# Kernel tuning notes

Measured on AMD Instinct MI355X. Metric: run time of the kernel, lower is better.

Reference implementation:

```python
import jax, jax.numpy as jnp
import numpy as np

NUM_CLASSES = 80
STRIDES = (8, 16, 32)
PRE_TOP_K = 1000
KEEP_TOP_K = 100
IOU_THR = 0.65
SCORE_THR = 0.25
CLASS_OFFSET = 8192.0  # > max image coordinate, separates classes for batched NMS


def _make_priors_strides(featmap_sizes):
    # MlvlPointGenerator.grid_priors with offset=0 (RTMDet-style point priors)
    priors, strides = [], []
    for (h, w), s in zip(featmap_sizes, STRIDES):
        ys, xs = jnp.meshgrid(jnp.arange(h, dtype=jnp.float32) * s,
                              jnp.arange(w, dtype=jnp.float32) * s, indexing='ij')
        priors.append(jnp.stack([xs.reshape(-1), ys.reshape(-1)], axis=-1))
        strides.append(jnp.full((h * w,), float(s), dtype=jnp.float32))
    return jnp.concatenate(priors, 0), jnp.concatenate(strides, 0)


def _flatten(x, c):
    # [B, C, H, W] -> [B, H*W, c] matching permute(0,2,3,1).reshape
    b = x.shape[0]
    return jnp.transpose(x, (0, 2, 3, 1)).reshape(b, -1, c)


def _iou_matrix(boxes):
    # boxes [K, 4] x1y1x2y2 -> pairwise IoU [K, K]
    area = jnp.maximum(boxes[:, 2] - boxes[:, 0], 0.0) * jnp.maximum(boxes[:, 3] - boxes[:, 1], 0.0)
    lt = jnp.maximum(boxes[:, None, :2], boxes[None, :, :2])
    rb = jnp.minimum(boxes[:, None, 2:], boxes[None, :, 2:])
    wh = jnp.maximum(rb - lt, 0.0)
    inter = wh[..., 0] * wh[..., 1]
    return inter / jnp.maximum(area[:, None] + area[None, :] - inter, 1e-6)


def _nms_single(boxes, scores, labels):
    # boxes [N,4], scores [N] (max over classes), labels [N] int32
    valid = scores > SCORE_THR
    scores = jnp.where(valid, scores, 0.0)
    top_scores, idx = jax.lax.top_k(scores, PRE_TOP_K)  # pre_top_k filtering
    b = boxes[idx]
    lab = labels[idx]
    val = valid[idx]
    # class-aware NMS via coordinate offset per class (batched_nms trick)
    off_boxes = b + (lab.astype(b.dtype) * CLASS_OFFSET)[:, None]
    iou = _iou_matrix(off_boxes)

    def body(suppressed, i):
        keep_i = ~suppressed[i]
        suppressed = suppressed | (keep_i & (iou[i] > IOU_THR))
        suppressed = suppressed.at[i].set(~keep_i)
        return suppressed, keep_i

    _, keeps = jax.lax.scan(body, ~val, jnp.arange(PRE_TOP_K))
    final_scores = jnp.where(keeps, top_scores, 0.0)
    fs, fidx = jax.lax.top_k(final_scores, KEEP_TOP_K)
    dets = jnp.concatenate([b[fidx], fs[:, None]], axis=-1)  # [keep_top_k, 5]
    return dets, lab[fidx]


def setup_inputs() -> dict:
    key = jax.random.key(0)
    ks = jax.random.split(key, 6)
    B, C = 16, NUM_CLASSES
    return {
        'cls0': jax.random.normal(ks[0], (B, C, 80, 80), jnp.float32),
        'cls1': jax.random.normal(ks[1], (B, C, 40, 40), jnp.float32),
        'cls2': jax.random.normal(ks[2], (B, C, 20, 20), jnp.float32),
        'box0': jax.random.uniform(ks[3], (B, 4, 80, 80), jnp.float32),
        'box1': jax.random.uniform(ks[4], (B, 4, 40, 40), jnp.float32),
        'box2': jax.random.uniform(ks[5], (B, 4, 20, 20), jnp.float32),
    }


def reference(cls0, cls1, cls2, box0, box1, box2):
    featmap_sizes = [c.shape[2:] for c in (cls0, cls1, cls2)]
    priors, strides = _make_priors_strides(featmap_sizes)  # [A,2], [A]
    scores = jax.nn.sigmoid(
        jnp.concatenate([_flatten(c, NUM_CLASSES) for c in (cls0, cls1, cls2)], axis=1))  # [B,A,C]
    preds = jnp.concatenate([_flatten(b, 4) for b in (box0, box1, box2)], axis=1)  # [B,A,4]
    # rtmdet_bbox_decoder: distances * stride around point priors
    d = preds * strides[None, :, None]
    x1 = priors[None, :, 0] - d[..., 0]
    y1 = priors[None, :, 1] - d[..., 1]
    x2 = priors[None, :, 0] + d[..., 2]
    y2 = priors[None, :, 1] + d[..., 3]
    bboxes = jnp.stack([x1, y1, x2, y2], axis=-1)  # [B,A,4]
    max_scores = jnp.max(scores, axis=-1)
    labels = jnp.argmax(scores, axis=-1).astype(jnp.int32)
    dets, out_labels = jax.vmap(_nms_single)(bboxes, max_scores, labels)
    return dets, out_labels
```

## Files before the change

### kernel.cpp

```cpp
#include <hip/hip_runtime.h>
#include <math.h>
#include <stdint.h>

typedef unsigned long long u64;
typedef unsigned int u32;

#define NCLS 80
#define NA   8400
#define NB   16
#define PRE_K 1000
#define M_FAST 256


__global__ __launch_bounds__(256) void k_decode(
    const float* __restrict__ cls0, const float* __restrict__ cls1,
    const float* __restrict__ cls2, const float* __restrict__ box0,
    const float* __restrict__ box1, const float* __restrict__ box2,
    u64* __restrict__ f_keys, float4* __restrict__ boxes,
    int* __restrict__ labels)
{
    __shared__ float pm0[3][64], pm1[3][64];
    __shared__ int   pl0[3][64], pl1[3][64];

    int t  = threadIdx.x & 63;
    int q  = threadIdx.x >> 6;
    int pa = blockIdx.x * 64 + t;
    int b  = blockIdx.y;
    bool act = pa < 4200;

    const float *clsp = cls0, *boxp = box0;
    int Wd = 80, s = 8, HW = 6400, hw = 0;
    float m0 = -1e30f, m1 = -1e30f;
    int lab0 = q * 20, lab1 = q * 20;

    if (act) {
        if (pa < 3200)      { clsp = cls0; boxp = box0; Wd = 80; s = 8;  HW = 6400; hw = 2 * pa; }
        else if (pa < 4000) { clsp = cls1; boxp = box1; Wd = 40; s = 16; HW = 1600; hw = 2 * pa - 6400; }
        else                { clsp = cls2; boxp = box2; Wd = 20; s = 32; HW = 400;  hw = 2 * pa - 8000; }

        const float* cp = clsp + (size_t)b * NCLS * HW + (size_t)(q * 20) * HW + hw;
        float2 v = *(const float2*)cp;
        m0 = v.x; m1 = v.y;
#pragma unroll
        for (int c = 1; c < 20; ++c) {
            float2 vv = *(const float2*)(cp + (size_t)c * HW);
            if (vv.x > m0) { m0 = vv.x; lab0 = q * 20 + c; }
            if (vv.y > m1) { m1 = vv.y; lab1 = q * 20 + c; }
        }
        if (q > 0) {
            pm0[q - 1][t] = m0; pl0[q - 1][t] = lab0;
            pm1[q - 1][t] = m1; pl1[q - 1][t] = lab1;
        }
    }
    __syncthreads();
    if (!act) return;
    int a = 2 * pa;

    if (q == 0) {
#pragma unroll
        for (int k = 0; k < 3; ++k) {
            float a0 = pm0[k][t]; if (a0 > m0) { m0 = a0; lab0 = pl0[k][t]; }
            float a1 = pm1[k][t]; if (a1 > m1) { m1 = a1; lab1 = pl1[k][t]; }
        }
        double e0 = exp(-(double)m0), e1 = exp(-(double)m1);
        float sc0 = (float)(1.0 / (1.0 + e0));
        float sc1 = (float)(1.0 / (1.0 + e1));
        float sz0 = (sc0 > 0.25f) ? sc0 : 0.0f;
        float sz1 = (sc1 > 0.25f) ? sc1 : 0.0f;
        u64* fkp = f_keys + (size_t)b * NA + a;
        fkp[0] = ((u64)__float_as_uint(sz0) << 32) | (u64)(~(u32)a);
        fkp[1] = ((u64)__float_as_uint(sz1) << 32) | (u64)(~(u32)(a + 1));
        int2 lt; lt.x = lab0; lt.y = lab1;
        *(int2*)(labels + (size_t)b * NA + a) = lt;
    } else if (q == 1) {
        const float* bp = boxp + (size_t)b * 4 * HW + hw;
        float fs = (float)s;
        float2 q0v = *(const float2*)(bp);
        float2 q1v = *(const float2*)(bp + HW);
        float2 q2v = *(const float2*)(bp + 2 * HW);
        float2 q3v = *(const float2*)(bp + 3 * HW);
        float px = (float)((hw % Wd) * s);
        float py = (float)((hw / Wd) * s);
        float px1 = px + fs;
        boxes[(size_t)b * NA + a]     = make_float4(px  - q0v.x * fs, py - q1v.x * fs, px  + q2v.x * fs, py + q3v.x * fs);
        boxes[(size_t)b * NA + a + 1] = make_float4(px1 - q0v.y * fs, py - q1v.y * fs, px1 + q2v.y * fs, py + q3v.y * fs);
    }
}

__device__ __forceinline__ u64 iou_bits(float4 A, float aar,
                                        const float4* __restrict__ bj,
                                        const float* __restrict__ aj, int jmax)
{
    u64 bits = 0;
    for (int jj = 0; jj < jmax; ++jj) {
        float4 Bx = bj[jj];
        float sab = aj[jj];
        float lx = fmaxf(A.x, Bx.x), ly = fmaxf(A.y, Bx.y);
        float rx = fminf(A.z, Bx.z), ry = fminf(A.w, Bx.w);
        float ww = fmaxf(__fsub_rn(rx, lx), 0.0f);
        float hh = fmaxf(__fsub_rn(ry, ly), 0.0f);
        float inter = __fmul_rn(ww, hh);
        float uni = __fsub_rn(__fadd_rn(aar, sab), inter);
        if (inter > 0.65f * fmaxf(uni, 1e-6f)) bits |= (1ull << jj);
    }
    return bits;
}

__global__ __launch_bounds__(1024, 1) void k_post(
    const u64* __restrict__ f_keys, const float4* __restrict__ boxes,
    const int* __restrict__ labels, float* __restrict__ out)
{
    __shared__ __align__(16) char shm[65536];
    __shared__ __align__(16) u64 cbs[1024];
    __shared__ u32 wtot[16];
    __shared__ u32 s_total, s_B, s_kept;
    int tid = threadIdx.x, lane = tid & 63, wv = tid >> 6;
    int b = blockIdx.x;

    const u64* fk = f_keys + (size_t)b * NA;

    u64 kr[9];
#pragma unroll
    for (int k = 0; k < 9; ++k) {
        int i = tid + k * 1024;
        kr[k] = (i < NA) ? fk[i] : 0ull;
    }

    {
        u32* R  = (u32*)shm;
        u32* C  = (u32*)(shm + 16384);
        u64* BK = (u64*)(shm + 32768);

        for (int i = tid; i < 4096; i += 1024) { R[i] = 0; C[i] = 0; }
        __syncthreads();

#pragma unroll
        for (int k = 0; k < 9; ++k) {
            u32 sb = (u32)(kr[k] >> 32);
            if (sb) {
                int bin = (int)(sb >> 12) - 0x3E800;
                bin = max(0, min(bin, 4095));
                atomicAdd(&R[bin], 1u);
            }
        }
        __syncthreads();

        u32 h0 = R[4*tid], h1 = R[4*tid+1], h2 = R[4*tid+2], h3 = R[4*tid+3];
        u32 g = h0 + h1 + h2 + h3;
        u32 S = g;
#pragma unroll
        for (int off = 1; off < 64; off <<= 1) {
            u32 x = __shfl_down(S, off, 64);
            if (lane + off < 64) S += x;
        }
        if (lane == 0) wtot[wv] = S;
        __syncthreads();
        u32 wsuf = 0;
#pragma unroll
        for (int w = 0; w < 16; ++w) if (w > wv) wsuf += wtot[w];
        u32 above = (S - g) + wsuf;
        u32 r3 = h3 + above, r2 = h2 + r3, r1 = h1 + r2, r0 = h0 + r1;
        R[4*tid] = r0; R[4*tid+1] = r1; R[4*tid+2] = r2; R[4*tid+3] = r3;
        if (tid == 0) s_total = 0;
        __syncthreads();
        if (tid == 0) s_total = R[0];
        __syncthreads();
        u32 total = s_total;

        if (tid == 0 && total < PRE_K) s_B = 0;
#pragma unroll
        for (int k = 0; k < 4; ++k) {
            int bin = 4*tid + k;
            u32 Rb = R[bin];
            u32 Rn = (bin < 4095) ? R[bin + 1] : 0;
            if (Rb >= PRE_K && Rn < PRE_K) s_B = (u32)bin;
        }
        __syncthreads();
        u32 B = s_B;
        u32 Cv = R[B];

        if (Cv <= 4096) {
#pragma unroll
            for (int k = 0; k < 9; ++k) {
                u64 key = kr[k];
                u32 sb = (u32)(key >> 32);
                if (sb) {
                    int bin = (int)(sb >> 12) - 0x3E800;
                    bin = max(0, min(bin, 4095));
                    if ((u32)bin >= B) {
                        u32 base = (bin < 4095) ? R[bin + 1] : 0;
                        u32 off = atomicAdd(&C[bin], 1u);
                        BK[base + off] = key;
                    }
                }
            }
            __syncthreads();
            for (int s2 = tid; s2 < (int)Cv; s2 += 1024) {
                u64 key = BK[s2];
                u32 sb = (u32)(key >> 32);
                int bin = (int)(sb >> 12) - 0x3E800;
                bin = max(0, min(bin, 4095));
                u32 base = (bin < 4095) ? R[bin + 1] : 0;
                u32 n = R[bin] - base;
                u32 cnt = 0;
                for (u32 j = 0; j < n; ++j) cnt += (BK[base + j] > key) ? 1u : 0u;
                u32 rank = base + cnt;
                if (rank < PRE_K) cbs[rank] = key;
            }
        } else {
            for (int i = tid; i < NA; i += 1024) {
                u64 key = fk[i];
                u32 sb = (u32)(key >> 32);
                if (!sb) continue;
                int bin = (int)(sb >> 12) - 0x3E800;
                bin = max(0, min(bin, 4095));
                if ((u32)bin < B) continue;
                u32 rank = 0;
                for (int j = 0; j < NA; ++j) rank += (fk[j] > key) ? 1u : 0u;
                if (rank < PRE_K) cbs[rank] = key;
            }
        }
        for (int t2 = tid; (int)total + t2 < PRE_K; t2 += 1024)
            cbs[total + t2] = (u64)(~(u32)t2);
        __syncthreads();
    }

    float4* sbox = (float4*)shm;
    float*  sar  = (float*)(shm + 16384);
    u64*    mk   = (u64*)(shm + 20480);
    u64*    Ksh  = (u64*)(shm + 28672);
    int*    chgA = (int*)(shm + 28928);

    if (tid < M_FAST) {
        u64 key = cbs[tid];
        u32 a = ~(u32)key;
        float4 bx = boxes[(size_t)b * NA + a];
        float off = (float)labels[(size_t)b * NA + a] * 8192.0f;
        float x1 = bx.x + off, y1 = bx.y + off, x2 = bx.z + off, y2 = bx.w + off;
        sbox[tid] = make_float4(x1, y1, x2, y2);
        float w = fmaxf(__fsub_rn(x2, x1), 0.0f);
        float h = fmaxf(__fsub_rn(y2, y1), 0.0f);
        sar[tid] = __fmul_rn(w, h);
    }
    __syncthreads();

    {
        int i = tid & 255, w = tid >> 8;
        u64 bits = 0;
        int iw = i >> 6;
        if (w <= iw) {
            int jmax = (w < iw) ? 64 : (i & 63);
            bits = iou_bits(sbox[i], sar[i], sbox + w * 64, sar + w * 64, jmax);
        }
        mk[i * 4 + w] = bits;
    }
    __syncthreads();

    bool inr = tid < M_FAST;
    u64 key = (tid < PRE_K) ? cbs[tid] : 0ull;
    bool valid = inr && ((u32)(key >> 32) != 0u);
    u64 rowm4[4];
#pragma unroll
    for (int k = 0; k < 4; ++k) rowm4[k] = inr ? mk[tid * 4 + k] : 0ull;

    u64 v0 = __ballot(valid);
    if (inr && lane == 0) Ksh[wv] = v0;
    if (tid < 32) chgA[tid] = 0;
    __syncthreads();

    int fin = 0;
    for (int it = 0; it < M_FAST + 2; ++it) {
        int p = it & 1;
        const u64* Kc = Ksh + p * 4;
        u64 kold = inr ? Kc[wv] : 0ull;
        u64 acc = 0;
#pragma unroll
        for (int k = 0; k < 4; ++k) acc |= rowm4[k] & Kc[k];
        bool kept = valid && (acc == 0ull);
        u64 nk = __ballot(kept);
        if (inr && lane == 0) {
            Ksh[(p ^ 1) * 4 + wv] = nk;
            if (nk != kold) chgA[it & 31] = 1;
        }
        __syncthreads();
        fin = p ^ 1;
        if (chgA[it & 31] == 0) break;
        if ((it & 31) == 31) {
            __syncthreads();
            if (tid < 32) chgA[tid] = 0;
            __syncthreads();
        }
    }
    const u64* Kf = Ksh + fin * 4;
    if (tid == 0) {
        u32 kt = 0;
#pragma unroll
        for (int k = 0; k < 4; ++k) kt += __popcll(Kf[k]);
        s_kept = kt;
    }
    __syncthreads();

    if (s_kept >= 100) {
        if (inr) {
            bool kept = (Kf[wv] >> lane) & 1ull;
            u64 low = (1ull << lane) - 1ull;
            int pc = 0;
#pragma unroll
            for (int k = 0; k < 4; ++k) {
                u64 lt = (k < wv) ? ~0ull : ((k == wv) ? low : 0ull);
                pc += __popcll(Kf[k] & lt);
            }
            if (kept && pc < 100) {
                u32 a = ~(u32)key;
                float4 bx = boxes[(size_t)b * NA + a];
                int lab = labels[(size_t)b * NA + a];
                float fsc = __uint_as_float((u32)(key >> 32));
                float* dr = out + (size_t)(b * 100 + pc) * 5;
                dr[0] = bx.x; dr[1] = bx.y; dr[2] = bx.z; dr[3] = bx.w; dr[4] = fsc;
                out[(size_t)NB * 100 * 5 + b * 100 + pc] = (float)lab;
            }
        }
        return;
    }

    {
        if (tid >= M_FAST && tid < PRE_K) {
            u64 kk = cbs[tid];
            u32 a = ~(u32)kk;
            float4 bx = boxes[(size_t)b * NA + a];
            float off = (float)labels[(size_t)b * NA + a] * 8192.0f;
            float x1 = bx.x + off, y1 = bx.y + off, x2 = bx.z + off, y2 = bx.w + off;
            sbox[tid] = make_float4(x1, y1, x2, y2);
            float w = fmaxf(__fsub_rn(x2, x1), 0.0f);
            float h = fmaxf(__fsub_rn(y2, y1), 0.0f);
            sar[tid] = __fmul_rn(w, h);
        }
        __syncthreads();

        bool inrF = tid < PRE_K;
        u64 rowm[16];
#pragma unroll
        for (int k = 0; k < 16; ++k) rowm[k] = 0ull;
        if (inrF) {
            float4 A = sbox[tid];
            float aar = sar[tid];
            for (int k = 0; k <= wv; ++k) {
                int jmax = (k < wv) ? 64 : lane;
                rowm[k] = iou_bits(A, aar, sbox + k * 64, sar + k * 64, jmax);
            }
        }
        bool valid2 = inrF && ((u32)(key >> 32) != 0u);

        u64 vF = __ballot(valid2);
        if (lane == 0) Ksh[wv] = vF;
        if (tid < 32) chgA[tid] = 0;
        __syncthreads();

        int finF = 0;
        for (int it = 0; it < PRE_K + 2; ++it) {
            int p = it & 1;
            const u64* Kc = Ksh + p * 16;
            u64 kold = Kc[wv];
            u64 acc = 0;
#pragma unroll
            for (int k = 0; k < 16; ++k) acc |= rowm[k] & Kc[k];
            bool kept = valid2 && (acc == 0ull);
            u64 nk = __ballot(kept);
            if (lane == 0) {
                Ksh[(p ^ 1) * 16 + wv] = nk;
                if (nk != kold) chgA[it & 31] = 1;
            }
            __syncthreads();
            finF = p ^ 1;
            if (chgA[it & 31] == 0) break;
            if ((it & 31) == 31) {
                __syncthreads();
                if (tid < 32) chgA[tid] = 0;
                __syncthreads();
            }
        }
        const u64* Kf2 = Ksh + finF * 16;

        u64 low = (1ull << lane) - 1ull;
        int pc = 0, Kt = 0;
#pragma unroll
        for (int k = 0; k < 16; ++k) {
            u64 kk = Kf2[k];
            u64 lt = (k < wv) ? ~0ull : ((k == wv) ? low : 0ull);
            pc += __popcll(kk & lt);
            Kt += __popcll(kk);
        }
        if (inrF) {
            bool kept = (Kf2[wv] >> lane) & 1ull;
            int row = kept ? pc : (Kt + (tid - pc));
            if (row < 100) {
                u32 a = ~(u32)key;
                float4 bx = boxes[(size_t)b * NA + a];
                int lab = labels[(size_t)b * NA + a];
                float fsc = kept ? __uint_as_float((u32)(key >> 32)) : 0.0f;
                float* dr = out + (size_t)(b * 100 + row) * 5;
                dr[0] = bx.x; dr[1] = bx.y; dr[2] = bx.z; dr[3] = bx.w; dr[4] = fsc;
                out[(size_t)NB * 100 * 5 + b * 100 + row] = (float)lab;
            }
        }
    }
}

extern "C" void kernel_launch(void* const* d_in, const int* in_sizes, int n_in,
                              void* d_out, int out_size, void* d_ws, size_t ws_size,
                              hipStream_t stream) {
    const float* cls0 = (const float*)d_in[0];
    const float* cls1 = (const float*)d_in[1];
    const float* cls2 = (const float*)d_in[2];
    const float* box0 = (const float*)d_in[3];
    const float* box1 = (const float*)d_in[4];
    const float* box2 = (const float*)d_in[5];
    float* out = (float*)d_out;

    char* w = (char*)d_ws;
    u64*    f_keys = (u64*)(w);
    float4* boxes  = (float4*)(w + 1075200);
    int*    labels = (int*)(w + 3225600);

    k_decode<<<dim3(66, NB), 256, 0, stream>>>(cls0, cls1, cls2, box0, box1, box2,
                                               f_keys, boxes, labels);
    k_post<<<NB, 1024, 0, stream>>>(f_keys, boxes, labels, out);
}
```

Before: 106.6 us.

## Fuse decode and NMS into one launch with flag-based inter-block handoff

Merges the decode and post-processing kernels into a single launch: per image, 17 blocks decode anchors and publish a completion flag, while one consumer block spins on those flags before running top-k and NMS. Labels are packed into the low bits of the sort key (index<<7 | label), so the labels buffer and its gathers go away. This removes a kernel launch boundary and some global traffic. In exchange it depends on consumer and producer blocks being co-resident. It also relies on a magic-value flag that is never reset, so a stale MAGIC from a previous call in the workspace could let the consumer read unfinished data.

```diff
diff --git a/kernel.cpp b/kernel.cpp
--- a/kernel.cpp
+++ b/kernel.cpp
@@ -10,112 +10,111 @@
 #define NB   16
 #define PRE_K 1000
 #define M_FAST 256
-
-
-__global__ __launch_bounds__(256) void k_decode(
+#define CHUNKS 17
+#define MAGIC  0x13579BDF2468ACE1ull
+
+
+__global__ __launch_bounds__(1024) void k_fused(
     const float* __restrict__ cls0, const float* __restrict__ cls1,
     const float* __restrict__ cls2, const float* __restrict__ box0,
     const float* __restrict__ box1, const float* __restrict__ box2,
     u64* __restrict__ f_keys, float4* __restrict__ boxes,
-    int* __restrict__ labels)
-{
-    __shared__ float pm0[3][64], pm1[3][64];
-    __shared__ int   pl0[3][64], pl1[3][64];
-
-    int t  = threadIdx.x & 63;
-    int q  = threadIdx.x >> 6;
-    int pa = blockIdx.x * 64 + t;
-    int b  = blockIdx.y;
-    bool act = pa < 4200;
-
-    const float *clsp = cls0, *boxp = box0;
-    int Wd = 80, s = 8, HW = 6400, hw = 0;
-    float m0 = -1e30f, m1 = -1e30f;
-    int lab0 = q * 20, lab1 = q * 20;
-
-    if (act) {
-        if (pa < 3200)      { clsp = cls0; boxp = box0; Wd = 80; s = 8;  HW = 6400; hw = 2 * pa; }
-        else if (pa < 4000) { clsp = cls1; boxp = box1; Wd = 40; s = 16; HW = 1600; hw = 2 * pa - 6400; }
-        else                { clsp = cls2; boxp = box2; Wd = 20; s = 32; HW = 400;  hw = 2 * pa - 8000; }
-
-        const float* cp = clsp + (size_t)b * NCLS * HW + (size_t)(q * 20) * HW + hw;
-        float2 v = *(const float2*)cp;
-        m0 = v.x; m1 = v.y;
-#pragma unroll
-        for (int c = 1; c < 20; ++c) {
-            float2 vv = *(const float2*)(cp + (size_t)c * HW);
-            if (vv.x > m0) { m0 = vv.x; lab0 = q * 20 + c; }
-            if (vv.y > m1) { m1 = vv.y; lab1 = q * 20 + c; }
-        }
-        if (q > 0) {
-            pm0[q - 1][t] = m0; pl0[q - 1][t] = lab0;
-            pm1[q - 1][t] = m1; pl1[q - 1][t] = lab1;
-        }
-    }
-    __syncthreads();
-    if (!act) return;
-    int a = 2 * pa;
-
-    if (q == 0) {
-#pragma unroll
-        for (int k = 0; k < 3; ++k) {
-            float a0 = pm0[k][t]; if (a0 > m0) { m0 = a0; lab0 = pl0[k][t]; }
-            float a1 = pm1[k][t]; if (a1 > m1) { m1 = a1; lab1 = pl1[k][t]; }
-        }
-        double e0 = exp(-(double)m0), e1 = exp(-(double)m1);
-        float sc0 = (float)(1.0 / (1.0 + e0));
-        float sc1 = (float)(1.0 / (1.0 + e1));
-        float sz0 = (sc0 > 0.25f) ? sc0 : 0.0f;
-        float sz1 = (sc1 > 0.25f) ? sc1 : 0.0f;
-        u64* fkp = f_keys + (size_t)b * NA + a;
-        fkp[0] = ((u64)__float_as_uint(sz0) << 32) | (u64)(~(u32)a);
-        fkp[1] = ((u64)__float_as_uint(sz1) << 32) | (u64)(~(u32)(a + 1));
-        int2 lt; lt.x = lab0; lt.y = lab1;
-        *(int2*)(labels + (size_t)b * NA + a) = lt;
-    } else if (q == 1) {
-        const float* bp = boxp + (size_t)b * 4 * HW + hw;
-        float fs = (float)s;
-        float2 q0v = *(const float2*)(bp);
-        float2 q1v = *(const float2*)(bp + HW);
-        float2 q2v = *(const float2*)(bp + 2 * HW);
-        float2 q3v = *(const float2*)(bp + 3 * HW);
-        float px = (float)((hw % Wd) * s);
-        float py = (float)((hw / Wd) * s);
-        float px1 = px + fs;
-        boxes[(size_t)b * NA + a]     = make_float4(px  - q0v.x * fs, py - q1v.x * fs, px  + q2v.x * fs, py + q3v.x * fs);
-        boxes[(size_t)b * NA + a + 1] = make_float4(px1 - q0v.y * fs, py - q1v.y * fs, px1 + q2v.y * fs, py + q3v.y * fs);
-    }
-}
-
-__device__ __forceinline__ u64 iou_bits(float4 A, float aar,
-                                        const float4* __restrict__ bj,
-                                        const float* __restrict__ aj, int jmax)
-{
-    u64 bits = 0;
-    for (int jj = 0; jj < jmax; ++jj) {
-        float4 Bx = bj[jj];
-        float sab = aj[jj];
-        float lx = fmaxf(A.x, Bx.x), ly = fmaxf(A.y, Bx.y);
-        float rx = fminf(A.z, Bx.z), ry = fminf(A.w, Bx.w);
-        float ww = fmaxf(__fsub_rn(rx, lx), 0.0f);
-        float hh = fmaxf(__fsub_rn(ry, ly), 0.0f);
-        float inter = __fmul_rn(ww, hh);
-        float uni = __fsub_rn(__fadd_rn(aar, sab), inter);
-        if (inter > 0.65f * fmaxf(uni, 1e-6f)) bits |= (1ull << jj);
-    }
-    return bits;
-}
-
-__global__ __launch_bounds__(1024, 1) void k_post(
-    const u64* __restrict__ f_keys, const float4* __restrict__ boxes,
-    const int* __restrict__ labels, float* __restrict__ out)
+    u64* __restrict__ flags, float* __restrict__ out)
 {
     __shared__ __align__(16) char shm[65536];
     __shared__ __align__(16) u64 cbs[1024];
     __shared__ u32 wtot[16];
     __shared__ u32 s_total, s_B, s_kept;
     int tid = threadIdx.x, lane = tid & 63, wv = tid >> 6;
-    int b = blockIdx.x;
+    int b = blockIdx.y;
+
+    if (blockIdx.x != 0) {
+        int c  = blockIdx.x - 1;
+        int t  = tid & 255;
+        int q  = tid >> 8;
+        int pa = c * 256 + t;
+        bool act = pa < 4200;
+
+        float* pm0 = (float*)shm;
+        float* pm1 = (float*)(shm + 3072);
+        int*   pl0 = (int*)(shm + 6144);
+        int*   pl1 = (int*)(shm + 9216);
+
+        const float *clsp = cls0, *boxp = box0;
+        int Wd = 80, ss = 8, HW = 6400, hw = 0;
+        float m0 = -1e30f, m1 = -1e30f;
+        int lab0 = q * 20, lab1 = q * 20;
+
+        if (act) {
+            if (pa < 3200)      { clsp = cls0; boxp = box0; Wd = 80; ss = 8;  HW = 6400; hw = 2 * pa; }
+            else if (pa < 4000) { clsp = cls1; boxp = box1; Wd = 40; ss = 16; HW = 1600; hw = 2 * pa - 6400; }
+            else                { clsp = cls2; boxp = box2; Wd = 20; ss = 32; HW = 400;  hw = 2 * pa - 8000; }
+
+            const float* cp = clsp + (size_t)b * NCLS * HW + (size_t)(q * 20) * HW + hw;
+            float2 v = *(const float2*)cp;
+            m0 = v.x; m1 = v.y;
+#pragma unroll 5
+            for (int c2 = 1; c2 < 20; ++c2) {
+                float2 vv = *(const float2*)(cp + (size_t)c2 * HW);
+                if (vv.x > m0) { m0 = vv.x; lab0 = q * 20 + c2; }
+                if (vv.y > m1) { m1 = vv.y; lab1 = q * 20 + c2; }
+            }
+            if (q > 0) {
+                pm0[(q - 1) * 256 + t] = m0; pl0[(q - 1) * 256 + t] = lab0;
+                pm1[(q - 1) * 256 + t] = m1; pl1[(q - 1) * 256 + t] = lab1;
+            }
+        }
+        __syncthreads();
+        if (act) {
+            int a = 2 * pa;
+            if (q == 0) {
+#pragma unroll
+                for (int k = 0; k < 3; ++k) {
+                    float a0 = pm0[k * 256 + t]; if (a0 > m0) { m0 = a0; lab0 = pl0[k * 256 + t]; }
+                    float a1 = pm1[k * 256 + t]; if (a1 > m1) { m1 = a1; lab1 = pl1[k * 256 + t]; }
+                }
+                double e0 = exp(-(double)m0), e1 = exp(-(double)m1);
+                float sc0 = (float)(1.0 / (1.0 + e0));
+                float sc1 = (float)(1.0 / (1.0 + e1));
+                float sz0 = (sc0 > 0.25f) ? sc0 : 0.0f;
+                float sz1 = (sc1 > 0.25f) ? sc1 : 0.0f;
+                u32 lo0 = ~(((u32)a << 7) | (u32)lab0);
+                u32 lo1 = ~((((u32)(a + 1)) << 7) | (u32)lab1);
+                u64* fkp = f_keys + (size_t)b * NA + a;
+                fkp[0] = ((u64)__float_as_uint(sz0) << 32) | (u64)lo0;
+                fkp[1] = ((u64)__float_as_uint(sz1) << 32) | (u64)lo1;
+            } else if (q == 1) {
+                const float* bp = boxp + (size_t)b * 4 * HW + hw;
+                float fs = (float)ss;
+                float2 q0v = *(const float2*)(bp);
+                float2 q1v = *(const float2*)(bp + HW);
+                float2 q2v = *(const float2*)(bp + 2 * HW);
+                float2 q3v = *(const float2*)(bp + 3 * HW);
+                float px = (float)((hw % Wd) * ss);
+                float py = (float)((hw / Wd) * ss);
+                float px1 = px + fs;
+                boxes[(size_t)b * NA + a]     = make_float4(px  - q0v.x * fs, py - q1v.x * fs, px  + q2v.x * fs, py + q3v.x * fs);
+                boxes[(size_t)b * NA + a + 1] = make_float4(px1 - q0v.y * fs, py - q1v.y * fs, px1 + q2v.y * fs, py + q3v.y * fs);
+            }
+        }
+        __syncthreads();
+        if (tid == 0) {
+            __threadfence();
+            __hip_atomic_store(&flags[b * CHUNKS + c], MAGIC,
+                               __ATOMIC_RELAXED, __HIP_MEMORY_SCOPE_AGENT);
+        }
+        return;
+    }
+
+    if (tid == 0) {
+        for (int i = 0; i < CHUNKS; ++i) {
+            while (__hip_atomic_load(&flags[b * CHUNKS + i],
+                                     __ATOMIC_RELAXED, __HIP_MEMORY_SCOPE_AGENT) != MAGIC)
+                __builtin_amdgcn_s_sleep(8);
+        }
+        __threadfence();
+    }
+    __syncthreads();
 
     const u64* fk = f_keys + (size_t)b * NA;
 
@@ -221,7 +220,7 @@
             }
         }
         for (int t2 = tid; (int)total + t2 < PRE_K; t2 += 1024)
-            cbs[total + t2] = (u64)(~(u32)t2);
+            cbs[total + t2] = (u64)(u32)~((u32)t2 << 7);
         __syncthreads();
     }
 
@@ -233,9 +232,10 @@
 
     if (tid < M_FAST) {
         u64 key = cbs[tid];
-        u32 a = ~(u32)key;
+        u32 v = ~(u32)key;
+        u32 a = v >> 7;
         float4 bx = boxes[(size_t)b * NA + a];
-        float off = (float)labels[(size_t)b * NA + a] * 8192.0f;
+        float off = (float)(v & 127u) * 8192.0f;
         float x1 = bx.x + off, y1 = bx.y + off, x2 = bx.z + off, y2 = bx.w + off;
         sbox[tid] = make_float4(x1, y1, x2, y2);
         float w = fmaxf(__fsub_rn(x2, x1), 0.0f);
@@ -250,7 +250,21 @@
         int iw = i >> 6;
         if (w <= iw) {
             int jmax = (w < iw) ? 64 : (i & 63);
-            bits = iou_bits(sbox[i], sar[i], sbox + w * 64, sar + w * 64, jmax);
+            float4 A = sbox[i];
+            float aar = sar[i];
+            const float4* bj = sbox + w * 64;
+            const float*  aj = sar  + w * 64;
+            for (int jj = 0; jj < jmax; ++jj) {
+                float4 Bx = bj[jj];
+                float sab = aj[jj];
+                float lx = fmaxf(A.x, Bx.x), ly = fmaxf(A.y, Bx.y);
+                float rx = fminf(A.z, Bx.z), ry = fminf(A.w, Bx.w);
+                float ww = fmaxf(__fsub_rn(rx, lx), 0.0f);
+                float hh = fmaxf(__fsub_rn(ry, ly), 0.0f);
+                float inter = __fmul_rn(ww, hh);
+                float uni = __fsub_rn(__fadd_rn(aar, sab), inter);
+                if (inter > 0.65f * fmaxf(uni, 1e-6f)) bits |= (1ull << jj);
+            }
         }
         mk[i * 4 + w] = bits;
     }
@@ -311,13 +325,13 @@
                 pc += __popcll(Kf[k] & lt);
             }
             if (kept && pc < 100) {
-                u32 a = ~(u32)key;
+                u32 v = ~(u32)key;
+                u32 a = v >> 7;
                 float4 bx = boxes[(size_t)b * NA + a];
-                int lab = labels[(size_t)b * NA + a];
                 float fsc = __uint_as_float((u32)(key >> 32));
                 float* dr = out + (size_t)(b * 100 + pc) * 5;
                 dr[0] = bx.x; dr[1] = bx.y; dr[2] = bx.z; dr[3] = bx.w; dr[4] = fsc;
-                out[(size_t)NB * 100 * 5 + b * 100 + pc] = (float)lab;
+                out[(size_t)NB * 100 * 5 + b * 100 + pc] = (float)(v & 127u);
             }
         }
         return;
@@ -326,9 +340,10 @@
     {
         if (tid >= M_FAST && tid < PRE_K) {
             u64 kk = cbs[tid];
-            u32 a = ~(u32)kk;
+            u32 v = ~(u32)kk;
+            u32 a = v >> 7;
             float4 bx = boxes[(size_t)b * NA + a];
-            float off = (float)labels[(size_t)b * NA + a] * 8192.0f;
+            float off = (float)(v & 127u) * 8192.0f;
             float x1 = bx.x + off, y1 = bx.y + off, x2 = bx.z + off, y2 = bx.w + off;
             sbox[tid] = make_float4(x1, y1, x2, y2);
             float w = fmaxf(__fsub_rn(x2, x1), 0.0f);
@@ -346,7 +361,21 @@
             float aar = sar[tid];
             for (int k = 0; k <= wv; ++k) {
                 int jmax = (k < wv) ? 64 : lane;
-                rowm[k] = iou_bits(A, aar, sbox + k * 64, sar + k * 64, jmax);
+                const float4* bj = sbox + k * 64;
+                const float*  aj = sar  + k * 64;
+                u64 bits = 0;
+                for (int jj = 0; jj < jmax; ++jj) {
+                    float4 Bx = bj[jj];
+                    float sab = aj[jj];
+                    float lx = fmaxf(A.x, Bx.x), ly = fmaxf(A.y, Bx.y);
+                    float rx = fminf(A.z, Bx.z), ry = fminf(A.w, Bx.w);
+                    float ww = fmaxf(__fsub_rn(rx, lx), 0.0f);
+                    float hh = fmaxf(__fsub_rn(ry, ly), 0.0f);
+                    float inter = __fmul_rn(ww, hh);
+                    float uni = __fsub_rn(__fadd_rn(aar, sab), inter);
+                    if (inter > 0.65f * fmaxf(uni, 1e-6f)) bits |= (1ull << jj);
+                }
+                rowm[k] = bits;
             }
         }
         bool valid2 = inrF && ((u32)(key >> 32) != 0u);
@@ -394,13 +423,13 @@
             bool kept = (Kf2[wv] >> lane) & 1ull;
             int row = kept ? pc : (Kt + (tid - pc));
             if (row < 100) {
-                u32 a = ~(u32)key;
+                u32 v = ~(u32)key;
+                u32 a = v >> 7;
                 float4 bx = boxes[(size_t)b * NA + a];
-                int lab = labels[(size_t)b * NA + a];
                 float fsc = kept ? __uint_as_float((u32)(key >> 32)) : 0.0f;
                 float* dr = out + (size_t)(b * 100 + row) * 5;
                 dr[0] = bx.x; dr[1] = bx.y; dr[2] = bx.z; dr[3] = bx.w; dr[4] = fsc;
-                out[(size_t)NB * 100 * 5 + b * 100 + row] = (float)lab;
+                out[(size_t)NB * 100 * 5 + b * 100 + row] = (float)(v & 127u);
             }
         }
     }
@@ -420,9 +449,8 @@
     char* w = (char*)d_ws;
     u64*    f_keys = (u64*)(w);
     float4* boxes  = (float4*)(w + 1075200);
-    int*    labels = (int*)(w + 3225600);
-
-    k_decode<<<dim3(66, NB), 256, 0, stream>>>(cls0, cls1, cls2, box0, box1, box2,
-                                               f_keys, boxes, labels);
-    k_post<<<NB, 1024, 0, stream>>>(f_keys, boxes, labels, out);
+    u64*    flags  = (u64*)(w + 3225600);
+
+    k_fused<<<dim3(1 + CHUNKS, NB), 1024, 0, stream>>>(
+        cls0, cls1, cls2, box0, box1, box2, f_keys, boxes, flags, out);
 }
```

After: 117.0 us. +9.7%, slower.
